# Kernel optimization log

Measured on AMD Instinct MI355X. Metric: run time of the kernel, lower is better.

## Reference

```python
import jax, jax.numpy as jnp
import numpy as np

HEADS = 16
GRID_SIZE = 5      # efficient-KAN default
SPLINE_ORDER = 3   # efficient-KAN default


def _grid(in_features, dtype):
    # grid_range = [-1, 1]
    h = 2.0 / GRID_SIZE
    g = jnp.arange(-SPLINE_ORDER, GRID_SIZE + SPLINE_ORDER + 1, dtype=dtype) * h - 1.0
    return jnp.broadcast_to(g, (in_features, g.shape[0]))  # (in, G)


def _b_splines(x, grid):
    # x: (N, in), grid: (in, G); Cox-de Boor recursion
    xg = x[:, :, None]
    bases = ((xg >= grid[:, :-1]) & (xg < grid[:, 1:])).astype(x.dtype)
    for k in range(1, SPLINE_ORDER + 1):
        bases = ((xg - grid[:, :-(k + 1)]) / (grid[:, k:-1] - grid[:, :-(k + 1)]) * bases[:, :, :-1]
                 + (grid[:, k + 1:] - xg) / (grid[:, k + 1:] - grid[:, 1:-k]) * bases[:, :, 1:])
    return bases  # (N, in, GRID_SIZE + SPLINE_ORDER)


def _kan_linear(x, base_w, spline_w, spline_scaler):
    grid = _grid(x.shape[-1], x.dtype)
    base = jax.nn.silu(x) @ base_w.T                      # (N, out)
    b = _b_splines(x, grid)                               # (N, in, K)
    sw = spline_w * spline_scaler[..., None]              # (out, in, K)
    return base + jnp.einsum('nik,oik->no', b, sw)


def setup_inputs():
    key = jax.random.key(0)
    S, H = 2048, 1024
    hd = H // HEADS
    K = GRID_SIZE + SPLINE_ORDER
    ks = jax.random.split(key, 6)
    x = jax.random.normal(ks[0], (S, H), jnp.float32)
    base_w = jax.random.normal(ks[1], (3 * H, H), jnp.float32) / np.float32(np.sqrt(H))
    spline_w = jax.random.normal(ks[2], (3 * H, H, K), jnp.float32) * 0.1
    spline_scaler = 1.0 + 0.1 * jax.random.normal(ks[3], (3 * H, H), jnp.float32)
    out_w = jax.random.normal(ks[4], (H, H), jnp.float32) / np.float32(np.sqrt(H))
    out_b = jnp.zeros((H,), jnp.float32)
    # RoPE rotation matrix (unit complex), theta = 10000
    t = jnp.arange(S, dtype=jnp.float32)
    freqs = 1.0 / (10000.0 ** (jnp.arange(0, hd, 2, dtype=jnp.float32) / hd))
    ang = jnp.outer(t, freqs)  # (S, hd//2)
    return {"x": x, "base_w": base_w, "spline_w": spline_w,
            "spline_scaler": spline_scaler, "out_w": out_w, "out_b": out_b,
            "rot_cos": jnp.cos(ang), "rot_sin": jnp.sin(ang)}


def reference(x, base_w, spline_w, spline_scaler, out_w, out_b, rot_cos, rot_sin):
    S, H = x.shape
    hd = H // HEADS
    qkv = _kan_linear(x, base_w, spline_w, spline_scaler)          # (S, 3H)
    qkv = qkv.reshape(1, S, HEADS, 3 * hd).transpose(0, 2, 1, 3)   # (1,h,S,3d)
    q, k, v = jnp.split(qkv, 3, axis=-1)                           # each (1,h,S,d)

    def rope(t):
        tp = t.reshape(1, HEADS, S, hd // 2, 2)
        c = rot_cos[None, None]
        s = rot_sin[None, None]
        re = tp[..., 0] * c - tp[..., 1] * s
        im = tp[..., 0] * s + tp[..., 1] * c
        return jnp.stack([re, im], axis=-1).reshape(1, HEADS, S, hd)

    q, k = rope(q), rope(k)
    scores = jnp.einsum('bhqd,bhkd->bhqk', q, k) / np.float32(np.sqrt(hd))
    attn = jax.nn.softmax(scores, axis=-1)
    ctx = jnp.einsum('bhqk,bhkd->bhqd', attn, v)
    ctx = ctx.transpose(0, 2, 1, 3).reshape(1, S, H)
    return ctx @ out_w.T + out_b
```

## Files before the change

### kernel.cpp

```cpp
#include <hip/hip_runtime.h>

typedef unsigned short u16;
typedef __bf16 bf16x8 __attribute__((ext_vector_type(8)));
typedef float f32x4 __attribute__((ext_vector_type(4)));

#define S_LEN 2048
#define NHEADS 16
#define HD 64
#define HDIM 1024
#define QKVN 3072
#define KAUG 9216

__device__ __forceinline__ u16 f2bf(float f) {
  union { float f; unsigned u; } v; v.f = f;
  unsigned r = v.u + 0x7fffu + ((v.u >> 16) & 1u);
  return (u16)(r >> 16);
}

typedef __attribute__((address_space(1))) const unsigned int gas_u32;
typedef __attribute__((address_space(3))) unsigned int las_u32;
__device__ __forceinline__ void gload_lds16(const void* g, void* l) {
  __builtin_amdgcn_global_load_lds((gas_u32*)g, (las_u32*)l, 16, 0, 0);
}

__global__ void prep_a_kernel(const float* __restrict__ x, u16* __restrict__ Aaug) {
  int idx = blockIdx.x * 256 + threadIdx.x;
  int n = idx >> 10, i = idx & 1023;
  float xv = x[idx];
  float sil = xv / (1.0f + __expf(-xv));
  Aaug[(size_t)n * KAUG + i] = f2bf(sil);

  float b[11];
#pragma unroll
  for (int j = 0; j < 11; ++j) {
    float t0 = 0.4f * (float)(j - 3) - 1.0f;
    float t1 = 0.4f * (float)(j - 2) - 1.0f;
    b[j] = (xv >= t0 && xv < t1) ? 1.0f : 0.0f;
  }
#pragma unroll
  for (int k = 1; k <= 3; ++k) {
    const float invk = (k == 1) ? 2.5f : (k == 2) ? 1.25f : 0.83333333f;
#pragma unroll
    for (int j = 0; j < 10; ++j) {
      if (j + k < 11) {
        float tj   = 0.4f * (float)(j - 3) - 1.0f;
        float tjk1 = 0.4f * (float)(j + k - 2) - 1.0f;
        b[j] = ((xv - tj) * b[j] + (tjk1 - xv) * b[j + 1]) * invk;
      }
    }
  }
  u16 t[8];
#pragma unroll
  for (int j = 0; j < 8; ++j) t[j] = f2bf(b[j]);
  uint4 pk;
  pk.x = (unsigned)t[0] | ((unsigned)t[1] << 16);
  pk.y = (unsigned)t[2] | ((unsigned)t[3] << 16);
  pk.z = (unsigned)t[4] | ((unsigned)t[5] << 16);
  pk.w = (unsigned)t[6] | ((unsigned)t[7] << 16);
  *reinterpret_cast<uint4*>(&Aaug[(size_t)n * KAUG + 1024 + i * 8]) = pk;
}

__global__ void prep_w_kernel(const float* __restrict__ bw, const float* __restrict__ sw,
                              const float* __restrict__ sc, u16* __restrict__ Waug) {
  int idx = blockIdx.x * 256 + threadIdx.x;
  int o = idx >> 10, i = idx & 1023;
  Waug[(size_t)o * KAUG + i] = f2bf(bw[idx]);
  float s = sc[idx];
  const float4* sp = reinterpret_cast<const float4*>(sw + (size_t)idx * 8);
  float4 a = sp[0], b = sp[1];
  uint4 pk;
  pk.x = (unsigned)f2bf(a.x * s) | ((unsigned)f2bf(a.y * s) << 16);
  pk.y = (unsigned)f2bf(a.z * s) | ((unsigned)f2bf(a.w * s) << 16);
  pk.z = (unsigned)f2bf(b.x * s) | ((unsigned)f2bf(b.y * s) << 16);
  pk.w = (unsigned)f2bf(b.z * s) | ((unsigned)f2bf(b.w * s) << 16);
  *reinterpret_cast<uint4*>(&Waug[(size_t)o * KAUG + 1024 + i * 8]) = pk;
}

__global__ void prep_ow_kernel(const float* __restrict__ ow, u16* __restrict__ owbf) {
  int idx = blockIdx.x * 256 + threadIdx.x;
  float4 v = reinterpret_cast<const float4*>(ow)[idx];
  uint2 pk;
  pk.x = (unsigned)f2bf(v.x) | ((unsigned)f2bf(v.y) << 16);
  pk.y = (unsigned)f2bf(v.z) | ((unsigned)f2bf(v.w) << 16);
  reinterpret_cast<uint2*>(owbf)[idx] = pk;
}

__global__ __launch_bounds__(256) void gemm_bt(
    const u16* __restrict__ A, const u16* __restrict__ B, float* __restrict__ C,
    int M, int N, int K, int Ksp)
{
  __shared__ u16 As[128 * 64];
  __shared__ u16 Bs[128 * 64];
  const int tid = threadIdx.x;
  const int lane = tid & 63;
  const int w = tid >> 6;
  const int wr = w >> 1, wc = w & 1;
  const int row0 = blockIdx.y * 128, col0 = blockIdx.x * 128;
  const int lr = lane & 15, lg = lane >> 4;
  const int kbeg = blockIdx.z * Ksp;
  const int nsteps = Ksp >> 6;
  float* Cz = C + (size_t)blockIdx.z * M * N;

  f32x4 acc[4][4];
#pragma unroll
  for (int m = 0; m < 4; ++m)
#pragma unroll
    for (int n = 0; n < 4; ++n) acc[m][n] = (f32x4){0.f, 0.f, 0.f, 0.f};

  const int srow = tid >> 3;
  const int c8sw = (tid & 7) ^ (srow & 7);
  const u16* ga = A + (size_t)(row0 + srow) * K + kbeg + c8sw * 8;
  const u16* gb = B + (size_t)(col0 + srow) * K + kbeg + c8sw * 8;
  const size_t rstep = (size_t)32 * K;
  const int xr = lr & 7;

  for (int ks = 0; ks < nsteps; ++ks) {
#pragma unroll
    for (int i = 0; i < 4; ++i) {
      gload_lds16(ga + i * rstep, &As[i * 2048 + tid * 8]);
      gload_lds16(gb + i * rstep, &Bs[i * 2048 + tid * 8]);
    }
    ga += 64; gb += 64;
    __syncthreads();

#pragma unroll
    for (int kk = 0; kk < 2; ++kk) {
      bf16x8 af[4], bf[4];
#pragma unroll
      for (int m = 0; m < 4; ++m) {
        int r = wr * 64 + m * 16 + lr;
        int ch = (kk * 4 + lg) ^ xr;
        af[m] = *reinterpret_cast<const bf16x8*>(&As[r * 64 + ch * 8]);
      }
#pragma unroll
      for (int n = 0; n < 4; ++n) {
        int r = wc * 64 + n * 16 + lr;
        int ch = (kk * 4 + lg) ^ xr;
        bf[n] = *reinterpret_cast<const bf16x8*>(&Bs[r * 64 + ch * 8]);
      }
#pragma unroll
      for (int m = 0; m < 4; ++m)
#pragma unroll
        for (int n = 0; n < 4; ++n)
          acc[m][n] = __builtin_amdgcn_mfma_f32_16x16x32_bf16(af[m], bf[n], acc[m][n], 0, 0, 0);
    }
    __syncthreads();
  }

#pragma unroll
  for (int m = 0; m < 4; ++m) {
    int row = row0 + wr * 64 + m * 16 + lg * 4;
#pragma unroll
    for (int n = 0; n < 4; ++n) {
      int col = col0 + wc * 64 + n * 16 + lr;
#pragma unroll
      for (int j = 0; j < 4; ++j)
        Cz[(size_t)(row + j) * N + col] = acc[m][n][j];
    }
  }
}

__global__ void reduce4_bias_kernel(const float* __restrict__ p, const float* __restrict__ bias,
                                    float* __restrict__ out) {
  int idx = blockIdx.x * 256 + threadIdx.x;
  const float4* p4 = reinterpret_cast<const float4*>(p);
  const size_t stride4 = (size_t)2048 * 1024 / 4;
  float4 a = p4[idx], b = p4[idx + stride4], c = p4[idx + 2 * stride4], d = p4[idx + 3 * stride4];
  float4 bv = reinterpret_cast<const float4*>(bias)[idx & 255];
  float4 r;
  r.x = a.x + b.x + c.x + d.x + bv.x;
  r.y = a.y + b.y + c.y + d.y + bv.y;
  r.z = a.z + b.z + c.z + d.z + bv.z;
  r.w = a.w + b.w + c.w + d.w + bv.w;
  reinterpret_cast<float4*>(out)[idx] = r;
}

__global__ void rope_kernel(const float* __restrict__ qkv0, const float* __restrict__ qkv1,
                            const float* __restrict__ rc, const float* __restrict__ rs,
                            u16* __restrict__ qro, u16* __restrict__ kro) {
  int idx = blockIdx.x * 256 + threadIdx.x;
  int h = idx >> 16;
  int rem = idx & 65535;
  int s = rem >> 5, i = rem & 31;
  size_t boff = (size_t)s * QKVN + h * 192 + 2 * i;
  float2 q0v = *reinterpret_cast<const float2*>(qkv0 + boff);
  float2 q1v = *reinterpret_cast<const float2*>(qkv1 + boff);
  float2 k0v = *reinterpret_cast<const float2*>(qkv0 + boff + 64);
  float2 k1v = *reinterpret_cast<const float2*>(qkv1 + boff + 64);
  float q0 = q0v.x + q1v.x, q1 = q0v.y + q1v.y;
  float k0 = k0v.x + k1v.x, k1 = k0v.y + k1v.y;
  float c = rc[s * 32 + i], sn = rs[s * 32 + i];
  size_t ob = ((size_t)(h * S_LEN + s)) * HD + 2 * i;
  unsigned qpk = (unsigned)f2bf((q0 * c - q1 * sn) * 0.125f) |
                 ((unsigned)f2bf((q0 * sn + q1 * c) * 0.125f) << 16);
  unsigned kpk = (unsigned)f2bf(k0 * c - k1 * sn) |
                 ((unsigned)f2bf(k0 * sn + k1 * c) << 16);
  *reinterpret_cast<unsigned*>(qro + ob) = qpk;
  *reinterpret_cast<unsigned*>(kro + ob) = kpk;
}

__global__ void vtrans_kernel(const float* __restrict__ qkv0, const float* __restrict__ qkv1,
                              u16* __restrict__ vT) {
  __shared__ float tile[64][65];
  int h = blockIdx.x >> 5;
  int st = blockIdx.x & 31;
  int s0 = st * 64;
  int t = threadIdx.x;
  int r = t >> 2, c4 = t & 3;
  size_t soff = (size_t)(s0 + r) * QKVN + h * 192 + 128 + c4 * 16;
  const float* src0 = qkv0 + soff;
  const float* src1 = qkv1 + soff;
#pragma unroll
  for (int z = 0; z < 4; ++z) {
    float4 v = *reinterpret_cast<const float4*>(src0 + z * 4);
    float4 u = *reinterpret_cast<const float4*>(src1 + z * 4);
    tile[r][c4 * 16 + z * 4 + 0] = v.x + u.x;
    tile[r][c4 * 16 + z * 4 + 1] = v.y + u.y;
    tile[r][c4 * 16 + z * 4 + 2] = v.z + u.z;
    tile[r][c4 * 16 + z * 4 + 3] = v.w + u.w;
  }
  __syncthreads();
  int d = t >> 2, sc = t & 3;
  u16* dst = vT + ((size_t)(h * 64 + d)) * S_LEN + s0 + sc * 16;
  unsigned wv[8];
#pragma unroll
  for (int z = 0; z < 8; ++z) {
    unsigned lo = f2bf(tile[sc * 16 + 2 * z][d]);
    unsigned hi = f2bf(tile[sc * 16 + 2 * z + 1][d]);
    wv[z] = lo | (hi << 16);
  }
  *reinterpret_cast<uint4*>(dst)     = make_uint4(wv[0], wv[1], wv[2], wv[3]);
  *reinterpret_cast<uint4*>(dst + 8) = make_uint4(wv[4], wv[5], wv[6], wv[7]);
}

__global__ __launch_bounds__(256) void attn_kernel(
    const u16* __restrict__ qro, const u16* __restrict__ kro,
    const u16* __restrict__ vT, u16* __restrict__ ctxb)
{
  __shared__ u16 plds[4][2][16 * 32];
  const int lane = threadIdx.x & 63;
  const int w = threadIdx.x >> 6;
  const int bid = (blockIdx.x & 7) * 64 + (blockIdx.x >> 3);
  const int h = bid >> 5;
  const int qt = (bid & 31) * 4 + w;
  const int lr = lane & 15, lg = lane >> 4;

  const u16* qbase = qro + ((size_t)(h * S_LEN + qt * 16 + lr)) * HD + lg * 8;
  bf16x8 qa0 = *reinterpret_cast<const bf16x8*>(qbase);
  bf16x8 qa1 = *reinterpret_cast<const bf16x8*>(qbase + 32);

  float mrow[4], lrow[4];
  f32x4 o[4];
#pragma unroll
  for (int j = 0; j < 4; ++j) { mrow[j] = -3.0e38f; lrow[j] = 0.f; }
#pragma unroll
  for (int n = 0; n < 4; ++n) o[n] = (f32x4){0.f, 0.f, 0.f, 0.f};

  for (int kt = 0; kt < 64; ++kt) {
    const int key0 = kt * 32;
    const u16* kb = kro + ((size_t)(h * S_LEN + key0 + lr)) * HD + lg * 8;
    bf16x8 k00 = *reinterpret_cast<const bf16x8*>(kb);
    bf16x8 k01 = *reinterpret_cast<const bf16x8*>(kb + 32);
    bf16x8 k10 = *reinterpret_cast<const bf16x8*>(kb + (size_t)16 * HD);
    bf16x8 k11 = *reinterpret_cast<const bf16x8*>(kb + (size_t)16 * HD + 32);

    f32x4 s0 = (f32x4){0.f, 0.f, 0.f, 0.f};
    f32x4 s1 = (f32x4){0.f, 0.f, 0.f, 0.f};
    __builtin_amdgcn_s_setprio(1);
    s0 = __builtin_amdgcn_mfma_f32_16x16x32_bf16(qa0, k00, s0, 0, 0, 0);
    s0 = __builtin_amdgcn_mfma_f32_16x16x32_bf16(qa1, k01, s0, 0, 0, 0);
    s1 = __builtin_amdgcn_mfma_f32_16x16x32_bf16(qa0, k10, s1, 0, 0, 0);
    s1 = __builtin_amdgcn_mfma_f32_16x16x32_bf16(qa1, k11, s1, 0, 0, 0);
    __builtin_amdgcn_s_setprio(0);

    float p0[4], p1[4], alpha[4];
#pragma unroll
    for (int j = 0; j < 4; ++j) {
      float v = fmaxf(s0[j], s1[j]);
      v = fmaxf(v, __shfl_xor(v, 1));
      v = fmaxf(v, __shfl_xor(v, 2));
      v = fmaxf(v, __shfl_xor(v, 4));
      v = fmaxf(v, __shfl_xor(v, 8));
      float mn = fmaxf(mrow[j], v);
      float al = __expf(mrow[j] - mn);
      float e0 = __expf(s0[j] - mn);
      float e1 = __expf(s1[j] - mn);
      lrow[j] = lrow[j] * al + e0 + e1;
      mrow[j] = mn;
      alpha[j] = al;
      p0[j] = e0; p1[j] = e1;
    }
#pragma unroll
    for (int n = 0; n < 4; ++n) {
#pragma unroll
      for (int j = 0; j < 4; ++j) o[n][j] *= alpha[j];
    }

    u16* pb = &plds[w][kt & 1][0];
#pragma unroll
    for (int j = 0; j < 4; ++j) {
      pb[(lg * 4 + j) * 32 + lr]      = f2bf(p0[j]);
      pb[(lg * 4 + j) * 32 + 16 + lr] = f2bf(p1[j]);
    }

    bf16x8 pa = *reinterpret_cast<const bf16x8*>(&pb[lr * 32 + lg * 8]);
    const u16* vb = vT + ((size_t)(h * 64 + lr)) * S_LEN + key0 + lg * 8;
    __builtin_amdgcn_s_setprio(1);
#pragma unroll
    for (int n = 0; n < 4; ++n) {
      bf16x8 vf = *reinterpret_cast<const bf16x8*>(vb + (size_t)(n * 16) * S_LEN);
      o[n] = __builtin_amdgcn_mfma_f32_16x16x32_bf16(pa, vf, o[n], 0, 0, 0);
    }
    __builtin_amdgcn_s_setprio(0);
  }

#pragma unroll
  for (int j = 0; j < 4; ++j) {
    float t = lrow[j];
    t += __shfl_xor(t, 1);
    t += __shfl_xor(t, 2);
    t += __shfl_xor(t, 4);
    t += __shfl_xor(t, 8);
    lrow[j] = 1.0f / t;
  }

#pragma unroll
  for (int n = 0; n < 4; ++n) {
    int col = h * 64 + n * 16 + lr;
#pragma unroll
    for (int j = 0; j < 4; ++j) {
      int row = qt * 16 + lg * 4 + j;
      ctxb[(size_t)row * HDIM + col] = f2bf(o[n][j] * lrow[j]);
    }
  }
}

extern "C" void kernel_launch(void* const* d_in, const int* in_sizes, int n_in,
                              void* d_out, int out_size, void* d_ws, size_t ws_size,
                              hipStream_t stream) {
  const float* x   = (const float*)d_in[0];
  const float* bw  = (const float*)d_in[1];
  const float* sw  = (const float*)d_in[2];
  const float* ssc = (const float*)d_in[3];
  const float* ow  = (const float*)d_in[4];
  const float* ob  = (const float*)d_in[5];
  const float* rc  = (const float*)d_in[6];
  const float* rs  = (const float*)d_in[7];
  float* out = (float*)d_out;

  char* ws = (char*)d_ws;
  u16*   Aaug  = (u16*)(ws);
  u16*   Waug  = (u16*)(ws + 37748736);
  float* qkv0  = (float*)(ws + 94371840);
  float* qkv1  = (float*)(ws + 119537664);
  u16*   qro   = (u16*)(ws + 144703488);
  u16*   kro   = (u16*)(ws + 148897792);
  u16*   vT    = (u16*)(ws + 153092096);
  u16*   owbf  = (u16*)(ws + 157286400);
  u16*   ctxb  = (u16*)(ws + 94371840);
  float* part  = (float*)(ws + 119537664);

  prep_a_kernel<<<8192, 256, 0, stream>>>(x, Aaug);
  prep_w_kernel<<<12288, 256, 0, stream>>>(bw, sw, ssc, Waug);
  prep_ow_kernel<<<1024, 256, 0, stream>>>(ow, owbf);

  gemm_bt<<<dim3(24, 16, 2), 256, 0, stream>>>(Aaug, Waug, qkv0, 2048, 3072, 9216, 4608);

  rope_kernel<<<4096, 256, 0, stream>>>(qkv0, qkv1, rc, rs, qro, kro);
  vtrans_kernel<<<512, 256, 0, stream>>>(qkv0, qkv1, vT);

  attn_kernel<<<512, 256, 0, stream>>>(qro, kro, vT, ctxb);

  gemm_bt<<<dim3(8, 16, 4), 256, 0, stream>>>(ctxb, owbf, part, 2048, 1024, 1024, 256);
  reduce4_bias_kernel<<<2048, 256, 0, stream>>>(part, ob, out);
}
```

Baseline: 529.8 us.

## Halve GEMM k-tile and restructure attention softmax with transposed scores and lazy rescale

The GEMM drops from 64-wide to 32-wide k-steps and removes the XOR swizzle, shrinking LDS use but doubling the number of barriers per k and likely reintroducing LDS bank conflicts. The attention kernel computes S^T by swapping MFMA operands, so each lane owns one query row. That lets it replace per-row cross-lane max reductions with two shuffles and rescale the output only when the max grows by more than a threshold. It also forms the P operand with register shuffles instead of an LDS round-trip. The lazy rescale trades exactness of the running max for skipping exp and multiply work, relying on the bounded margin to avoid overflow.

```diff
diff --git a/kernel.cpp b/kernel.cpp
--- a/kernel.cpp
+++ b/kernel.cpp
@@ -89,8 +89,8 @@
     const u16* __restrict__ A, const u16* __restrict__ B, float* __restrict__ C,
     int M, int N, int K, int Ksp)
 {
-  __shared__ u16 As[128 * 64];
-  __shared__ u16 Bs[128 * 64];
+  __shared__ u16 As[128 * 32];
+  __shared__ u16 Bs[128 * 32];
   const int tid = threadIdx.x;
   const int lane = tid & 63;
   const int w = tid >> 6;
@@ -98,7 +98,7 @@
   const int row0 = blockIdx.y * 128, col0 = blockIdx.x * 128;
   const int lr = lane & 15, lg = lane >> 4;
   const int kbeg = blockIdx.z * Ksp;
-  const int nsteps = Ksp >> 6;
+  const int nsteps = Ksp >> 5;
   float* Cz = C + (size_t)blockIdx.z * M * N;
 
   f32x4 acc[4][4];
@@ -107,43 +107,36 @@
 #pragma unroll
     for (int n = 0; n < 4; ++n) acc[m][n] = (f32x4){0.f, 0.f, 0.f, 0.f};
 
-  const int srow = tid >> 3;
-  const int c8sw = (tid & 7) ^ (srow & 7);
-  const u16* ga = A + (size_t)(row0 + srow) * K + kbeg + c8sw * 8;
-  const u16* gb = B + (size_t)(col0 + srow) * K + kbeg + c8sw * 8;
-  const size_t rstep = (size_t)32 * K;
-  const int xr = lr & 7;
+  const int arow = tid >> 2;
+  const int kch  = tid & 3;
+  const u16* ga = A + (size_t)(row0 + arow) * K + kbeg + kch * 8;
+  const u16* gb = B + (size_t)(col0 + arow) * K + kbeg + kch * 8;
+  const size_t rstep = (size_t)64 * K;
 
   for (int ks = 0; ks < nsteps; ++ks) {
-#pragma unroll
-    for (int i = 0; i < 4; ++i) {
-      gload_lds16(ga + i * rstep, &As[i * 2048 + tid * 8]);
-      gload_lds16(gb + i * rstep, &Bs[i * 2048 + tid * 8]);
-    }
-    ga += 64; gb += 64;
+    gload_lds16(ga, &As[tid * 8]);
+    gload_lds16(ga + rstep, &As[2048 + tid * 8]);
+    gload_lds16(gb, &Bs[tid * 8]);
+    gload_lds16(gb + rstep, &Bs[2048 + tid * 8]);
+    ga += 32; gb += 32;
     __syncthreads();
 
-#pragma unroll
-    for (int kk = 0; kk < 2; ++kk) {
-      bf16x8 af[4], bf[4];
-#pragma unroll
-      for (int m = 0; m < 4; ++m) {
-        int r = wr * 64 + m * 16 + lr;
-        int ch = (kk * 4 + lg) ^ xr;
-        af[m] = *reinterpret_cast<const bf16x8*>(&As[r * 64 + ch * 8]);
-      }
-#pragma unroll
-      for (int n = 0; n < 4; ++n) {
-        int r = wc * 64 + n * 16 + lr;
-        int ch = (kk * 4 + lg) ^ xr;
-        bf[n] = *reinterpret_cast<const bf16x8*>(&Bs[r * 64 + ch * 8]);
-      }
-#pragma unroll
-      for (int m = 0; m < 4; ++m)
-#pragma unroll
-        for (int n = 0; n < 4; ++n)
-          acc[m][n] = __builtin_amdgcn_mfma_f32_16x16x32_bf16(af[m], bf[n], acc[m][n], 0, 0, 0);
-    }
+    bf16x8 af[4], bf[4];
+#pragma unroll
+    for (int m = 0; m < 4; ++m) {
+      int r = wr * 64 + m * 16 + lr;
+      af[m] = *reinterpret_cast<const bf16x8*>(&As[r * 32 + lg * 8]);
+    }
+#pragma unroll
+    for (int n = 0; n < 4; ++n) {
+      int r = wc * 64 + n * 16 + lr;
+      bf[n] = *reinterpret_cast<const bf16x8*>(&Bs[r * 32 + lg * 8]);
+    }
+#pragma unroll
+    for (int m = 0; m < 4; ++m)
+#pragma unroll
+      for (int n = 0; n < 4; ++n)
+        acc[m][n] = __builtin_amdgcn_mfma_f32_16x16x32_bf16(af[m], bf[n], acc[m][n], 0, 0, 0);
     __syncthreads();
   }
 
@@ -237,7 +230,6 @@
     const u16* __restrict__ qro, const u16* __restrict__ kro,
     const u16* __restrict__ vT, u16* __restrict__ ctxb)
 {
-  __shared__ u16 plds[4][2][16 * 32];
   const int lane = threadIdx.x & 63;
   const int w = threadIdx.x >> 6;
   const int bid = (blockIdx.x & 7) * 64 + (blockIdx.x >> 3);
@@ -249,12 +241,14 @@
   bf16x8 qa0 = *reinterpret_cast<const bf16x8*>(qbase);
   bf16x8 qa1 = *reinterpret_cast<const bf16x8*>(qbase + 32);
 
-  float mrow[4], lrow[4];
+  float mrow = -3.0e38f, lrow = 0.f;
   f32x4 o[4];
 #pragma unroll
-  for (int j = 0; j < 4; ++j) { mrow[j] = -3.0e38f; lrow[j] = 0.f; }
-#pragma unroll
   for (int n = 0; n < 4; ++n) o[n] = (f32x4){0.f, 0.f, 0.f, 0.f};
+
+  const int sA = lr + 32 * (lg & 1);
+  const int sB = sA + 16;
+  const bool loHalf = (lg < 2);
 
   for (int kt = 0; kt < 64; ++kt) {
     const int key0 = kt * 32;
@@ -267,62 +261,68 @@
     f32x4 s0 = (f32x4){0.f, 0.f, 0.f, 0.f};
     f32x4 s1 = (f32x4){0.f, 0.f, 0.f, 0.f};
     __builtin_amdgcn_s_setprio(1);
-    s0 = __builtin_amdgcn_mfma_f32_16x16x32_bf16(qa0, k00, s0, 0, 0, 0);
-    s0 = __builtin_amdgcn_mfma_f32_16x16x32_bf16(qa1, k01, s0, 0, 0, 0);
-    s1 = __builtin_amdgcn_mfma_f32_16x16x32_bf16(qa0, k10, s1, 0, 0, 0);
-    s1 = __builtin_amdgcn_mfma_f32_16x16x32_bf16(qa1, k11, s1, 0, 0, 0);
+    s0 = __builtin_amdgcn_mfma_f32_16x16x32_bf16(k00, qa0, s0, 0, 0, 0);
+    s0 = __builtin_amdgcn_mfma_f32_16x16x32_bf16(k01, qa1, s0, 0, 0, 0);
+    s1 = __builtin_amdgcn_mfma_f32_16x16x32_bf16(k10, qa0, s1, 0, 0, 0);
+    s1 = __builtin_amdgcn_mfma_f32_16x16x32_bf16(k11, qa1, s1, 0, 0, 0);
     __builtin_amdgcn_s_setprio(0);
 
-    float p0[4], p1[4], alpha[4];
+    float vmax = fmaxf(fmaxf(fmaxf(s0[0], s0[1]), fmaxf(s0[2], s0[3])),
+                       fmaxf(fmaxf(s1[0], s1[1]), fmaxf(s1[2], s1[3])));
+    vmax = fmaxf(vmax, __shfl_xor(vmax, 16));
+    vmax = fmaxf(vmax, __shfl_xor(vmax, 32));
+
+    if (__any(vmax > mrow + 8.0f)) {
+      float mnew = fmaxf(mrow, vmax);
+      float al = __expf(mrow - mnew);
+      float alO[4];
+#pragma unroll
+      for (int j = 0; j < 4; ++j) alO[j] = __shfl(al, lg * 4 + j);
+#pragma unroll
+      for (int n = 0; n < 4; ++n)
+#pragma unroll
+        for (int j = 0; j < 4; ++j) o[n][j] *= alO[j];
+      lrow *= al;
+      mrow = mnew;
+    }
+
+    float p[8];
 #pragma unroll
     for (int j = 0; j < 4; ++j) {
-      float v = fmaxf(s0[j], s1[j]);
-      v = fmaxf(v, __shfl_xor(v, 1));
-      v = fmaxf(v, __shfl_xor(v, 2));
-      v = fmaxf(v, __shfl_xor(v, 4));
-      v = fmaxf(v, __shfl_xor(v, 8));
-      float mn = fmaxf(mrow[j], v);
-      float al = __expf(mrow[j] - mn);
-      float e0 = __expf(s0[j] - mn);
-      float e1 = __expf(s1[j] - mn);
-      lrow[j] = lrow[j] * al + e0 + e1;
-      mrow[j] = mn;
-      alpha[j] = al;
-      p0[j] = e0; p1[j] = e1;
-    }
-#pragma unroll
-    for (int n = 0; n < 4; ++n) {
-#pragma unroll
-      for (int j = 0; j < 4; ++j) o[n][j] *= alpha[j];
-    }
-
-    u16* pb = &plds[w][kt & 1][0];
-#pragma unroll
-    for (int j = 0; j < 4; ++j) {
-      pb[(lg * 4 + j) * 32 + lr]      = f2bf(p0[j]);
-      pb[(lg * 4 + j) * 32 + 16 + lr] = f2bf(p1[j]);
-    }
-
-    bf16x8 pa = *reinterpret_cast<const bf16x8*>(&pb[lr * 32 + lg * 8]);
+      p[j]     = __expf(s0[j] - mrow);
+      p[4 + j] = __expf(s1[j] - mrow);
+    }
+    lrow += ((p[0] + p[1]) + (p[2] + p[3])) + ((p[4] + p[5]) + (p[6] + p[7]));
+
+    union { bf16x8 v; uint4 u; } pk_;
+#pragma unroll
+    for (int j = 0; j < 8; ++j) pk_.v[j] = (__bf16)p[j];
+
+    unsigned a0 = __shfl((int)pk_.u.x, sA), a1 = __shfl((int)pk_.u.y, sA);
+    unsigned a2 = __shfl((int)pk_.u.x, sB), a3 = __shfl((int)pk_.u.y, sB);
+    unsigned b0 = __shfl((int)pk_.u.z, sA), b1 = __shfl((int)pk_.u.w, sA);
+    unsigned b2 = __shfl((int)pk_.u.z, sB), b3 = __shfl((int)pk_.u.w, sB);
+    union { uint4 u; bf16x8 v; } pa_;
+    pa_.u.x = loHalf ? a0 : b0;
+    pa_.u.y = loHalf ? a1 : b1;
+    pa_.u.z = loHalf ? a2 : b2;
+    pa_.u.w = loHalf ? a3 : b3;
+
     const u16* vb = vT + ((size_t)(h * 64 + lr)) * S_LEN + key0 + lg * 8;
     __builtin_amdgcn_s_setprio(1);
 #pragma unroll
     for (int n = 0; n < 4; ++n) {
       bf16x8 vf = *reinterpret_cast<const bf16x8*>(vb + (size_t)(n * 16) * S_LEN);
-      o[n] = __builtin_amdgcn_mfma_f32_16x16x32_bf16(pa, vf, o[n], 0, 0, 0);
+      o[n] = __builtin_amdgcn_mfma_f32_16x16x32_bf16(pa_.v, vf, o[n], 0, 0, 0);
     }
     __builtin_amdgcn_s_setprio(0);
   }
 
-#pragma unroll
-  for (int j = 0; j < 4; ++j) {
-    float t = lrow[j];
-    t += __shfl_xor(t, 1);
-    t += __shfl_xor(t, 2);
-    t += __shfl_xor(t, 4);
-    t += __shfl_xor(t, 8);
-    lrow[j] = 1.0f / t;
-  }
+  lrow += __shfl_xor(lrow, 16);
+  lrow += __shfl_xor(lrow, 32);
+  float linv[4];
+#pragma unroll
+  for (int j = 0; j < 4; ++j) linv[j] = 1.0f / __shfl(lrow, lg * 4 + j);
 
 #pragma unroll
   for (int n = 0; n < 4; ++n) {
@@ -330,7 +330,7 @@
 #pragma unroll
     for (int j = 0; j < 4; ++j) {
       int row = qt * 16 + lg * 4 + j;
-      ctxb[(size_t)row * HDIM + col] = f2bf(o[n][j] * lrow[j]);
+      ctxb[(size_t)row * HDIM + col] = f2bf(o[n][j] * linv[j]);
     }
   }
 }
```

Result: faster. 499.5 us (-5.7%).
